# Kernel optimization log

Hardware: AMD Instinct MI355X
Metric: run time of the kernel (lower is better)

Reference implementation:

```python
import jax, jax.numpy as jnp
import numpy as np

DIM = 512
N = 64
DIV = 8
H = DIM // DIV  # 64
BATCH = 8
L_SEQ = 2048


def _kernel_dplr(Lam, P, B, C, step, L):
    # Lam: (N,) complex, P: (N,1), B: (N,H), C: (H,N), step: scalar
    omega = jnp.exp(-2j * jnp.pi * (jnp.arange(L) / L))        # (L,)
    g = (2.0 / step) * (1.0 - omega) / (1.0 + omega)           # (L,) generating-fn nodes
    c = 2.0 / (1.0 + omega)                                    # (L,)
    r = 1.0 / (g[:, None] - Lam[None, :])                      # (L,N) Cauchy resolvent
    Cc = jnp.conj(C)                                           # (H,N)
    p = P[:, 0]                                                # (N,)
    pc = jnp.conj(p)
    # vectorized Cauchy dot-products (torch version loops over L)
    k00 = jnp.einsum('in,nj,ln->lij', Cc, B, r)                # (L,H,H)
    k01 = jnp.einsum('in,n,ln->li', Cc, p, r)                  # (L,H)
    k10 = jnp.einsum('n,nj,ln->lj', pc, B, r)                  # (L,H)
    k11 = jnp.einsum('n,n,ln->l', pc, p, r)                    # (L,)
    # woodbury correction: inv(1 + k11) is a 1x1 batched inverse -> elementwise
    at_roots = c[:, None, None] * (
        k00 - k01[:, :, None] * (1.0 / (1.0 + k11))[:, None, None] * k10[:, None, :]
    )                                                          # (L,H,H)
    return jnp.fft.ifft(at_roots, n=L, axis=0).real            # (L,H,H)


def _fft_conv(u, K):
    # u: (b,L,H) real, K: (L,H,H) real. Linear conv via length-2L FFT.
    L = K.shape[0]
    ud = jnp.fft.rfft(u, n=2 * L, axis=1)                      # (b,Lf,H)
    Kd = jnp.fft.rfft(K, n=2 * L, axis=0)                      # (Lf,H,H)
    yf = jnp.einsum('lij,blj->bli', Kd, ud)                    # (b,Lf,H)
    return jnp.fft.irfft(yf, n=2 * L, axis=1)[:, :L]           # (b,L,H)


def reference(u, Lambda_re, Lambda_im, P_re, P_im, B_re, B_im, C_re, C_im, step):
    # straight-through clamp of Lambda_re (torch does an in-place no_grad clamp)
    Lambda_re = Lambda_re + jax.lax.stop_gradient(
        jnp.minimum(Lambda_re, -1e-4) - Lambda_re)
    Lam = Lambda_re + 1j * Lambda_im                           # (N,div)
    P = P_re + 1j * P_im                                       # (N,1,div)
    Bm = B_re + 1j * B_im                                      # (N,H,div)
    Cm = C_re + 1j * C_im                                      # (H,N,div)
    b, L, d = u.shape
    u4 = u.reshape(b, L, d // DIV, DIV)                        # (b,L,H,div)
    s = jnp.exp(step)[0]
    K = jax.vmap(_kernel_dplr, in_axes=(-1, -1, -1, -1, None, None),
                 out_axes=-1)(Lam, P, Bm, Cm, s, L)            # (L,H,H,div)
    y = jax.vmap(_fft_conv, in_axes=(-1, -1), out_axes=-1)(u4, K)  # (b,L,H,div)
    return y.reshape(b, L, d)


def setup_inputs() -> dict:
    key = jax.random.key(0)
    ks = jax.random.split(key, 10)
    sc = 0.5 ** 0.5
    u = jax.random.normal(ks[0], (BATCH, L_SEQ, DIM), dtype=jnp.float32)
    Lambda_re = -(jax.random.uniform(ks[1], (N, DIV), dtype=jnp.float32) * 0.5 + 0.1)
    Lambda_im = jax.random.normal(ks[2], (N, DIV), dtype=jnp.float32)
    P_re = jax.random.normal(ks[3], (N, 1, DIV), dtype=jnp.float32) * sc
    P_im = jax.random.normal(ks[4], (N, 1, DIV), dtype=jnp.float32) * sc
    B_re = jax.random.normal(ks[5], (N, H, DIV), dtype=jnp.float32) * sc
    B_im = jax.random.normal(ks[6], (N, H, DIV), dtype=jnp.float32) * sc
    C_re = jax.random.normal(ks[7], (H, N, DIV), dtype=jnp.float32) * sc
    C_im = jax.random.normal(ks[8], (H, N, DIV), dtype=jnp.float32) * sc
    step = jax.random.uniform(ks[9], (1,), dtype=jnp.float32,
                              minval=float(np.log(0.001)), maxval=float(np.log(0.1)))
    return {"u": u, "Lambda_re": Lambda_re, "Lambda_im": Lambda_im,
            "P_re": P_re, "P_im": P_im, "B_re": B_re, "B_im": B_im,
            "C_re": C_re, "C_im": C_im, "step": step}
```

## Files before the change

kernel.cpp:

```cpp
#include <hip/hip_runtime.h>
#include <hip/hip_bf16.h>
#include <math.h>

#define LSEQ 2048
#define NM   64
#define HD   64
#define NDIV 8
#define NB   8
#define NF   2049
#define ATROWS 4224

#define SL(E) ((E) + ((E) >> 5))
#define FFT_BUF 2112

typedef __attribute__((ext_vector_type(8))) short bf16x8;
typedef __attribute__((ext_vector_type(4))) float f32x4;

__device__ __forceinline__ unsigned pack_c(float2 v) {
  __hip_bfloat162 h = __float22bfloat162_rn(v);
  return *reinterpret_cast<unsigned*>(&h);
}
__device__ __forceinline__ float2 unpack_c(unsigned u) {
  __hip_bfloat162 h = *reinterpret_cast<__hip_bfloat162*>(&u);
  return __bfloat1622float2(h);
}
__device__ __forceinline__ unsigned short f2bf(float v) {
  __hip_bfloat16 h = __float2bfloat16(v);
  return *reinterpret_cast<unsigned short*>(&h);
}

struct cplxd { double x, y; };
__device__ __forceinline__ cplxd cmuld(cplxd a, cplxd b) {
  return {a.x*b.x - a.y*b.y, a.x*b.y + a.y*b.x};
}
__device__ __forceinline__ cplxd cdivd(cplxd a, cplxd b) {
  double inv = 1.0 / (b.x*b.x + b.y*b.y);
  return {(a.x*b.x + a.y*b.y)*inv, (a.y*b.x - a.x*b.y)*inv};
}

__device__ __forceinline__ void build_tw256(float2* TW) {
  int m = threadIdx.x;
  if (m < 256) {
    float s, c;
    __sincosf(-3.14159265358979324f * (float)m * (1.0f/512.0f), &s, &c);
    TW[m] = make_float2(c, s);
  }
}

template<int SIGN, int M>
__device__ __forceinline__ void r4_stage(const float2* __restrict__ src,
                                         float2* __restrict__ dst,
                                         const float2* __restrict__ TW) {
  constexpr int L = 2048 / (4 * M);
  __syncthreads();
  #pragma unroll
  for (int t = 0; t < 2; t++) {
    int idx = (int)threadIdx.x + t * 256;
    int q = idx / M;
    int p = idx & (M - 1);
    float2 a0 = src[SL(idx)];
    float2 a1 = src[SL(idx + 512)];
    float2 a2 = src[SL(idx + 1024)];
    float2 a3 = src[SL(idx + 1536)];
    float2 w = TW[(p * L) >> 1];
    float2 W1 = make_float2(w.x, (SIGN > 0) ? -w.y : w.y);
    float2 W2 = make_float2(W1.x*W1.x - W1.y*W1.y, 2.f*W1.x*W1.y);
    float2 W3 = make_float2(W2.x*W1.x - W2.y*W1.y, W2.x*W1.y + W2.y*W1.x);
    float2 b1 = make_float2(a1.x*W1.x - a1.y*W1.y, a1.x*W1.y + a1.y*W1.x);
    float2 b2 = make_float2(a2.x*W2.x - a2.y*W2.y, a2.x*W2.y + a2.y*W2.x);
    float2 b3 = make_float2(a3.x*W3.x - a3.y*W3.y, a3.x*W3.y + a3.y*W3.x);
    float2 e0 = make_float2(a0.x + b2.x, a0.y + b2.y);
    float2 e1 = make_float2(b1.x + b3.x, b1.y + b3.y);
    float2 d0 = make_float2(a0.x - b2.x, a0.y - b2.y);
    float2 d1 = make_float2(b1.x - b3.x, b1.y - b3.y);
    float2 o1, o3;
    if (SIGN < 0) { o1 = make_float2(d0.x + d1.y, d0.y - d1.x);
                    o3 = make_float2(d0.x - d1.y, d0.y + d1.x); }
    else          { o1 = make_float2(d0.x - d1.y, d0.y + d1.x);
                    o3 = make_float2(d0.x + d1.y, d0.y - d1.x); }
    int ob = q * 4 * M + p;
    dst[SL(ob)]         = make_float2(e0.x + e1.x, e0.y + e1.y);
    dst[SL(ob + M)]     = o1;
    dst[SL(ob + 2*M)]   = make_float2(e0.x - e1.x, e0.y - e1.y);
    dst[SL(ob + 3*M)]   = o3;
  }
}

template<int SIGN>
__device__ __forceinline__ void r4_mid(float2* a, float2* b, const float2* TW) {
  r4_stage<SIGN,   4>(a, b, TW);
  r4_stage<SIGN,  16>(b, a, TW);
  r4_stage<SIGN,  64>(a, b, TW);
  r4_stage<SIGN, 256>(b, a, TW);
}

template<int SIGN>
__device__ __forceinline__ void r2f_ldst(const float2* __restrict__ src,
                                         float2* __restrict__ dst) {
  __syncthreads();
  #pragma unroll
  for (int t = 0; t < 4; t++) {
    int p = (int)threadIdx.x + t * 256;
    float2 a = src[SL(p)], b = src[SL(p + 1024)];
    float s, c;
    __sincosf(-6.28318530717958647f * (float)p * (1.0f/2048.0f), &s, &c);
    float wy = (SIGN > 0) ? -s : s;
    float2 wb = make_float2(b.x*c - b.y*wy, b.x*wy + b.y*c);
    dst[SL(p)]        = make_float2(a.x + wb.x, a.y + wb.y);
    dst[SL(p + 1024)] = make_float2(a.x - wb.x, a.y - wb.y);
  }
}

__device__ __forceinline__ void r4g_bf16_inv(const unsigned* __restrict__ row,
                                             float2* __restrict__ dst) {
  #pragma unroll
  for (int t = 0; t < 2; t++) {
    int idx = (int)threadIdx.x + t * 256;
    float2 a0 = unpack_c(row[idx]);
    float2 a1 = unpack_c(row[idx + 512]);
    float2 a2 = unpack_c(row[idx + 1024]);
    float2 a3 = unpack_c(row[idx + 1536]);
    float2 e0 = make_float2(a0.x + a2.x, a0.y + a2.y);
    float2 e1 = make_float2(a1.x + a3.x, a1.y + a3.y);
    float2 d0 = make_float2(a0.x - a2.x, a0.y - a2.y);
    float2 d1 = make_float2(a1.x - a3.x, a1.y - a3.y);
    float2 o1 = make_float2(d0.x - d1.y, d0.y + d1.x);
    float2 o3 = make_float2(d0.x + d1.y, d0.y - d1.x);
    int ob = idx * 4;
    dst[SL(ob)]   = make_float2(e0.x + e1.x, e0.y + e1.y);
    dst[SL(ob+1)] = o1;
    dst[SL(ob+2)] = make_float2(e0.x - e1.x, e0.y - e1.y);
    dst[SL(ob+3)] = o3;
  }
}

__device__ __forceinline__ void r4g_f32pad_fwd(const float2* __restrict__ g,
                                               float2* __restrict__ dst) {
  #pragma unroll
  for (int t = 0; t < 2; t++) {
    int idx = (int)threadIdx.x + t * 256;
    float2 a0 = g[idx];
    float2 a1 = g[idx + 512];
    int ob = idx * 4;
    dst[SL(ob)]   = make_float2(a0.x + a1.x, a0.y + a1.y);
    dst[SL(ob+1)] = make_float2(a0.x + a1.y, a0.y - a1.x);
    dst[SL(ob+2)] = make_float2(a0.x - a1.x, a0.y - a1.y);
    dst[SL(ob+3)] = make_float2(a0.x - a1.y, a0.y + a1.x);
  }
}

__device__ __forceinline__ void r4_modstage(const float2* __restrict__ src,
                                            float2* __restrict__ dst) {
  __syncthreads();
  const float sc = 1.0f/2048.0f;
  const float R = 0.70710678118654752f;
  #pragma unroll
  for (int t = 0; t < 2; t++) {
    int idx = (int)threadIdx.x + t * 256;
    float k0 = src[SL(idx)].x        * sc;
    float k1 = src[SL(idx + 512)].x  * sc;
    float k2 = src[SL(idx + 1024)].x * sc;
    float k3 = src[SL(idx + 1536)].x * sc;
    float s, c;
    __sincosf(-3.14159265358979324f * (float)idx * (1.0f/2048.0f), &s, &c);
    float2 a0 = make_float2(k0*c,         k0*s);
    float2 a1 = make_float2(k1*R*(c + s), k1*R*(s - c));
    float2 a2 = make_float2(k2*s,        -k2*c);
    float2 a3 = make_float2(k3*R*(s - c), -k3*R*(s + c));
    float2 e0 = make_float2(a0.x + a2.x, a0.y + a2.y);
    float2 e1 = make_float2(a1.x + a3.x, a1.y + a3.y);
    float2 d0 = make_float2(a0.x - a2.x, a0.y - a2.y);
    float2 d1 = make_float2(a1.x - a3.x, a1.y - a3.y);
    float2 o1 = make_float2(d0.x + d1.y, d0.y - d1.x);
    float2 o3 = make_float2(d0.x - d1.y, d0.y + d1.x);
    int ob = idx * 4;
    dst[SL(ob)]   = make_float2(e0.x + e1.x, e0.y + e1.y);
    dst[SL(ob+1)] = o1;
    dst[SL(ob+2)] = make_float2(e0.x - e1.x, e0.y - e1.y);
    dst[SL(ob+3)] = o3;
  }
}

__device__ __forceinline__ void r2f_gw_bf16(const float2* __restrict__ src,
                                            unsigned* __restrict__ row) {
  __syncthreads();
  #pragma unroll
  for (int t = 0; t < 4; t++) {
    int p = (int)threadIdx.x + t * 256;
    float2 a = src[SL(p)], b = src[SL(p + 1024)];
    float s, c;
    __sincosf(-6.28318530717958647f * (float)p * (1.0f/2048.0f), &s, &c);
    float2 wb = make_float2(b.x*c - b.y*s, b.x*s + b.y*c);
    row[2*p + 1] = pack_c(make_float2(a.x + wb.x, a.y + wb.y));
  }
}

__device__ __forceinline__ void r2f_gw_f32h(const float2* __restrict__ src,
                                            float2* __restrict__ dst) {
  __syncthreads();
  const float sc = 1.0f/2048.0f;
  #pragma unroll
  for (int t = 0; t < 4; t++) {
    int p = (int)threadIdx.x + t * 256;
    float2 a = src[SL(p)], b = src[SL(p + 1024)];
    float s, c;
    __sincosf(-6.28318530717958647f * (float)p * (1.0f/2048.0f), &s, &c);
    float wy = -s;
    float2 wb = make_float2(b.x*c - b.y*wy, b.x*wy + b.y*c);
    dst[p] = make_float2((a.x + wb.x)*sc, (a.y + wb.y)*sc);
  }
}

__global__ __launch_bounds__(256) void ssm_kt(
    const float* __restrict__ Cre, const float* __restrict__ Cim,
    const float* __restrict__ Bre, const float* __restrict__ Bim,
    const float* __restrict__ Pre, const float* __restrict__ Pim,
    float2* __restrict__ CT, float2* __restrict__ BT, float2* __restrict__ PT) {
  int idx = blockIdx.x * 256 + threadIdx.x;
  int dv = idx >> 12, n = (idx >> 6) & 63, x = idx & 63;
  CT[idx] = make_float2(Cre[((size_t)x*NM + n)*NDIV + dv], -Cim[((size_t)x*NM + n)*NDIV + dv]);
  BT[idx] = make_float2(Bre[((size_t)n*HD + x)*NDIV + dv],  Bim[((size_t)n*HD + x)*NDIV + dv]);
  if (idx < NDIV*NM) {
    int dv2 = idx >> 6, n2 = idx & 63;
    PT[idx] = make_float2(Pre[n2*NDIV + dv2], Pim[n2*NDIV + dv2]);
  }
}

__global__ __launch_bounds__(256) void ssm_k0a(
    const float* __restrict__ Lre, const float* __restrict__ Lim,
    const float* __restrict__ Pre, const float* __restrict__ Pim,
    const float* __restrict__ step, unsigned short* __restrict__ RBr,
    unsigned short* __restrict__ RBi, float2* __restrict__ cpx) {
  int idx = blockIdx.x * 256 + threadIdx.x;
  int qn = idx & 3;
  int rest = idx >> 2;
  int l = rest & (LSEQ - 1);
  int dv = rest >> 11;
  double s = (double)expf(step[0]);
  float angf = -6.2831855f * ((float)l * (1.0f/2048.0f));
  double si, co;
  sincos((double)angf, &si, &co);
  cplxd om    = {co, si};
  cplxd one_p = {1.0 + om.x,  om.y};
  double ts = 2.0 / s;
  cplxd g = cdivd({ts*(1.0 - om.x), ts*(-om.y)}, one_p);
  cplxd c = cdivd({2.0, 0.0}, one_p);
  double k11x = 0.0, k11y = 0.0;
  for (int u = 0; u < 16; u++) {
    int n = qn*16 + u;
    float lre = fminf(Lre[n*NDIV+dv], -0.0001f);
    float lim = Lim[n*NDIV+dv];
    cplxd den = {g.x - (double)lre, g.y - (double)lim};
    cplxd r   = cdivd({1.0, 0.0}, den);
    cplxd rcv = cmuld(c, r);
    size_t bidx = (((size_t)(dv*8 + (n >> 3)))*LSEQ + l)*8 + (n & 7);
    RBr[bidx] = f2bf((float)rcv.x);
    RBi[bidx] = f2bf((float)rcv.y);
    double pr = (double)Pre[n*NDIV+dv], pi = (double)Pim[n*NDIV+dv];
    double p2 = pr*pr + pi*pi;
    k11x += p2 * rcv.x; k11y += p2 * rcv.y;
  }
  k11x += __shfl_xor(k11x, 1); k11y += __shfl_xor(k11y, 1);
  k11x += __shfl_xor(k11x, 2); k11y += __shfl_xor(k11y, 2);
  if (qn == 0)
    cpx[(size_t)dv*LSEQ + l] = make_float2((float)(c.x + k11x), (float)(c.y + k11y));
}

__global__ __launch_bounds__(256) void ssm_km(
    const float2* __restrict__ CT, const float2* __restrict__ BT,
    const float2* __restrict__ PT, unsigned short* __restrict__ ATr,
    unsigned short* __restrict__ ATi, unsigned short* __restrict__ ATin) {
  __shared__ float2 PAN[4096];
  __shared__ float2 ROW[64];
  int dv = blockIdx.y;
  int ib = blockIdx.x;
  int tid = threadIdx.x;
  if (ib < 64) {
    for (int q = tid; q < 4096; q += 256) PAN[q] = BT[(size_t)dv*4096 + q];
    if (tid < 64) ROW[tid] = CT[(size_t)dv*4096 + tid*64 + ib];
    __syncthreads();
    int j = tid >> 2, nq = tid & 3;
    size_t rbase = ((size_t)dv*ATROWS + ib*64 + j)*64;
    for (int u = 0; u < 16; u++) {
      int n = nq*16 + u;
      float2 cv = ROW[n];
      float2 bv = PAN[n*64 + j];
      float xr = cv.x*bv.x - cv.y*bv.y, xi = cv.x*bv.y + cv.y*bv.x;
      ATr[rbase + n] = f2bf(xr); ATi[rbase + n] = f2bf(xi); ATin[rbase + n] = f2bf(-xi);
    }
  } else {
    for (int q = tid; q < 4096; q += 256) PAN[q] = CT[(size_t)dv*4096 + q];
    if (tid < 64) ROW[tid] = PT[dv*64 + tid];
    __syncthreads();
    int x = tid >> 2, nq = tid & 3;
    size_t pbase = ((size_t)dv*ATROWS + 4096 + x)*64;
    for (int u = 0; u < 16; u++) {
      int n = nq*16 + u;
      float2 cv = PAN[n*64 + x];
      float2 pv = ROW[n];
      float xr = cv.x*pv.x - cv.y*pv.y, xi = cv.x*pv.y + cv.y*pv.x;
      ATr[pbase + n] = f2bf(xr); ATi[pbase + n] = f2bf(xi); ATin[pbase + n] = f2bf(-xi);
    }
    __syncthreads();
    for (int q = tid; q < 4096; q += 256) PAN[q] = BT[(size_t)dv*4096 + q];
    __syncthreads();
    size_t qbase = ((size_t)dv*ATROWS + 4160 + x)*64;
    for (int u = 0; u < 16; u++) {
      int n = nq*16 + u;
      float2 bv = PAN[n*64 + x];
      float2 pv = ROW[n];
      float xr = pv.x*bv.x + pv.y*bv.y, xi = pv.x*bv.y - pv.y*bv.x;
      ATr[qbase + n] = f2bf(xr); ATi[qbase + n] = f2bf(xi); ATin[qbase + n] = f2bf(-xi);
    }
  }
}

__device__ __forceinline__ void gemm_core(
    const unsigned short* __restrict__ ATr, const unsigned short* __restrict__ ATi,
    const unsigned short* __restrict__ ATin, const unsigned short* __restrict__ RBr,
    const unsigned short* __restrict__ RBi, int dv, int mrow0, int l0, int lane,
    f32x4 accR[4], f32x4 accI[4]) {
  int mloc = lane & 15, kgrp = lane >> 4;
  #pragma unroll
  for (int t = 0; t < 4; t++) {
    accR[t] = (f32x4){0.f, 0.f, 0.f, 0.f};
    accI[t] = (f32x4){0.f, 0.f, 0.f, 0.f};
  }
  size_t abase = ((size_t)dv*ATROWS + mrow0 + mloc)*64 + kgrp*8;
  #pragma unroll
  for (int s = 0; s < 2; s++) {
    bf16x8 ar = *reinterpret_cast<const bf16x8*>(ATr  + abase + s*32);
    bf16x8 ai = *reinterpret_cast<const bf16x8*>(ATi  + abase + s*32);
    bf16x8 an = *reinterpret_cast<const bf16x8*>(ATin + abase + s*32);
    size_t bbase = (((size_t)(dv*8 + s*4 + kgrp))*LSEQ + l0 + mloc)*8;
    #pragma unroll
    for (int t = 0; t < 4; t++) {
      bf16x8 br = *reinterpret_cast<const bf16x8*>(RBr + bbase + t*128);
      bf16x8 bi = *reinterpret_cast<const bf16x8*>(RBi + bbase + t*128);
      accR[t] = __builtin_amdgcn_mfma_f32_16x16x32_bf16(ar, br, accR[t], 0, 0, 0);
      accR[t] = __builtin_amdgcn_mfma_f32_16x16x32_bf16(an, bi, accR[t], 0, 0, 0);
      accI[t] = __builtin_amdgcn_mfma_f32_16x16x32_bf16(ar, bi, accI[t], 0, 0, 0);
      accI[t] = __builtin_amdgcn_mfma_f32_16x16x32_bf16(ai, br, accI[t], 0, 0, 0);
    }
  }
}

__global__ __launch_bounds__(256) void ssm_g1(
    const unsigned short* __restrict__ ATr, const unsigned short* __restrict__ ATi,
    const unsigned short* __restrict__ ATin, const unsigned short* __restrict__ RBr,
    const unsigned short* __restrict__ RBi, const float2* __restrict__ cpx,
    float2* __restrict__ A1h, float2* __restrict__ K10h) {
  int which = blockIdx.x;
  int nBlk = blockIdx.y;
  int dv = blockIdx.z;
  int wave = threadIdx.x >> 6, lane = threadIdx.x & 63;
  int mrow0 = 4096 + which*64 + wave*16;
  int l0 = nBlk * 64;
  f32x4 accR[4], accI[4];
  gemm_core(ATr, ATi, ATin, RBr, RBi, dv, mrow0, l0, lane, accR, accI);
  int rbase = (lane >> 4) * 4;
  #pragma unroll
  for (int t = 0; t < 4; t++) {
    int l = l0 + t*16 + (lane & 15);
    if (which == 0) {
      float2 w = cpx[((size_t)dv << 11) + l];
      float inv = 1.0f / (w.x*w.x + w.y*w.y);
      #pragma unroll
      for (int r = 0; r < 4; r++) {
        int x = wave*16 + rbase + r;
        float sx = accR[t][r], sy = accI[t][r];
        A1h[((size_t)(dv*64 + x))*LSEQ + l] =
            make_float2((sx*w.x + sy*w.y)*inv, (sy*w.x - sx*w.y)*inv);
      }
    } else {
      #pragma unroll
      for (int r = 0; r < 4; r++) {
        int x = wave*16 + rbase + r;
        K10h[((size_t)(dv*LSEQ + l))*64 + x] = make_float2(accR[t][r], accI[t][r]);
      }
    }
  }
}

__global__ __launch_bounds__(256) void ssm_g2(
    const unsigned short* __restrict__ ATr, const unsigned short* __restrict__ ATi,
    const unsigned short* __restrict__ ATin, const unsigned short* __restrict__ RBr,
    const unsigned short* __restrict__ RBi, const float2* __restrict__ A1h,
    const float2* __restrict__ K10h, unsigned* __restrict__ big, int dv) {
  int mBlk = blockIdx.x;
  int nBlk = blockIdx.y;
  int wave = threadIdx.x >> 6, lane = threadIdx.x & 63;
  int mrow0 = mBlk*64 + wave*16;
  int l0 = nBlk * 64;
  f32x4 accR[4], accI[4];
  gemm_core(ATr, ATi, ATin, RBr, RBi, dv, mrow0, l0, lane, accR, accI);
  int rbase = (lane >> 4) * 4;
  #pragma unroll
  for (int t = 0; t < 4; t++) {
    int l = l0 + t*16 + (lane & 15);
    float2 a1 = A1h[((size_t)(dv*64 + mBlk))*LSEQ + l];
    const float2* kp = K10h + ((size_t)(dv*LSEQ + l))*64 + wave*16 + rbase;
    #pragma unroll
    for (int r = 0; r < 4; r++) {
      float2 k10 = kp[r];
      float cx = a1.x*k10.x - a1.y*k10.y;
      float cy = a1.x*k10.y + a1.y*k10.x;
      int chain = mBlk*64 + wave*16 + rbase + r;
      big[(size_t)chain*NF + l] = pack_c(make_float2(accR[t][r] - cx, accI[t][r] - cy));
    }
  }
}

__global__ __launch_bounds__(256) void ssm_ku(const float* __restrict__ u, float* __restrict__ ut) {
  __shared__ float s[16][513];
  int b  = blockIdx.x >> 7;
  int l0 = (blockIdx.x & 127) << 4;
  int tid = threadIdx.x;
  for (int q = tid; q < 16*512; q += 256) {
    int ll = q >> 9, dd = q & 511;
    s[ll][dd] = u[((size_t)b*LSEQ + l0 + ll)*512 + dd];
  }
  __syncthreads();
  for (int q = tid; q < 16*512; q += 256) {
    int d = q >> 4, ll = q & 15;
    int dvv = d & 7, h = d >> 3;
    ut[(((size_t)(dvv*NB + b))*HD + h)*LSEQ + l0 + ll] = s[ll][d];
  }
}

__global__ __launch_bounds__(256) void ssm_k3(const float* __restrict__ ut, float2* __restrict__ ud, int dv) {
  __shared__ float2 b0[FFT_BUF];
  __shared__ float2 b1[FFT_BUF];
  __shared__ float2 TW[256];
  int tid = threadIdx.x;
  int c = blockIdx.x;
  const float2* src = (const float2*)(ut + ((size_t)dv*512 + c) * LSEQ);
  float2* dst = ud + (size_t)c * NF;
  build_tw256(TW);
  r4g_f32pad_fwd(src, b1);
  r4_mid<-1>(b1, b0, TW);
  r2f_ldst<-1>(b1, b0);
  __syncthreads();
  for (int f = tid; f <= 2048; f += 256) {
    int fa = f & 2047, fb = (2048 - f) & 2047;
    float2 Zf = b0[SL(fa)];
    float2 Zm = b0[SL(fb)];
    float Ex = (Zf.x + Zm.x)*0.5f, Ey = (Zf.y - Zm.y)*0.5f;
    float Dx = Zf.x - Zm.x,        Dy = Zf.y + Zm.y;
    float Ox = Dy*0.5f, Oy = -Dx*0.5f;
    float s, c2;
    __sincosf(-6.28318530717958647f * (float)f * (1.0f/4096.0f), &s, &c2);
    float WOx = Ox*c2 - Oy*s, WOy = Ox*s + Oy*c2;
    dst[f] = make_float2(Ex + WOx, Ey + WOy);
  }
}

__global__ __launch_bounds__(256) void ssm_k2(unsigned* __restrict__ big) {
  __shared__ float2 b0[FFT_BUF];
  __shared__ float2 b1[FFT_BUF];
  __shared__ float2 TW[256];
  int tid = threadIdx.x;
  unsigned* row = big + (size_t)blockIdx.x * NF;
  build_tw256(TW);
  float2 ev[4];
  #pragma unroll
  for (int k = 0; k < 4; k++) {
    int l = tid + 256*k;
    float2 a = unpack_c(row[l]);
    float2 b = unpack_c(row[(2048 - l) & 2047]);
    ev[k] = make_float2((a.x + b.x)*0.5f, (a.y - b.y)*0.5f);
  }
  float ev1024 = (tid == 0) ? unpack_c(row[1024]).x : 0.f;
  r4g_bf16_inv(row, b1);
  __syncthreads();
  #pragma unroll
  for (int k = 0; k < 4; k++) { int l = tid + 256*k; row[2*l] = pack_c(ev[k]); }
  if (tid == 0) row[2048] = pack_c(make_float2(ev1024, 0.f));
  r4_mid<1>(b1, b0, TW);
  r2f_ldst<1>(b1, b0);
  r4_modstage(b0, b1);
  r4_mid<-1>(b1, b0, TW);
  r2f_gw_bf16(b1, row);
}

__global__ __launch_bounds__(256) void ssm_k4(
    const unsigned* __restrict__ kdt, const float2* __restrict__ ud,
    float2* __restrict__ yf) {
  __shared__ float2 uds[NB][32][16];
  int tid = threadIdx.x;
  int f0 = blockIdx.x * 16;
  int i0 = blockIdx.y * 16;
  int ii = tid >> 4, ff = tid & 15;
  int i = i0 + ii;
  int f = f0 + ff;
  int fr = (f < NF) ? f : 2048;
  float2 acc[NB];
  #pragma unroll
  for (int b = 0; b < NB; b++) acc[b] = make_float2(0.f, 0.f);
  for (int jh = 0; jh < 2; jh++) {
    __syncthreads();
    for (int q = tid; q < NB*32*16; q += 256) {
      int b = q >> 9, j = (q >> 4) & 31, fq = q & 15;
      int f_ = f0 + fq;
      uds[b][j][fq] = (f_ < NF) ? ud[((size_t)(b*HD + jh*32 + j))*NF + f_]
                                : make_float2(0.f, 0.f);
    }
    __syncthreads();
    for (int j = 0; j < 32; j++) {
      float2 kv = unpack_c(kdt[((size_t)(i*HD + jh*32 + j))*NF + fr]);
      #pragma unroll
      for (int b = 0; b < NB; b++) {
        float2 uv = uds[b][j][ff];
        acc[b].x += kv.x*uv.x - kv.y*uv.y;
        acc[b].y += kv.x*uv.y + kv.y*uv.x;
      }
    }
  }
  if (f < NF) {
    #pragma unroll
    for (int b = 0; b < NB; b++)
      yf[((size_t)(b*HD + i))*NF + f] = acc[b];
  }
}

__global__ __launch_bounds__(256) void ssm_k5(const float2* __restrict__ yf,
                                              float* __restrict__ yt, int dv) {
  __shared__ float2 b0[FFT_BUF];
  __shared__ float2 b1[FFT_BUF];
  __shared__ float2 TW[256];
  int tid = threadIdx.x;
  int b = blockIdx.x >> 6, i = blockIdx.x & 63;
  const float2* src = yf + (size_t)(b*HD + i) * NF;
  float2* dst = (float2*)(yt + (((size_t)(dv*NB + b))*HD + i) * LSEQ);
  build_tw256(TW);
  for (int k = tid; k < 2048; k += 256) {
    float2 Xk = src[k];
    float2 Xm = src[2048 - k];
    float Ex = (Xk.x + Xm.x)*0.5f, Ey = (Xk.y - Xm.y)*0.5f;
    float Dx = Xk.x - Xm.x,        Dy = Xk.y + Xm.y;
    float s, c;
    __sincosf(6.28318530717958647f * (float)k * (1.0f/4096.0f), &s, &c);
    float Ox = 0.5f*(Dx*c - Dy*s);
    float Oy = 0.5f*(Dx*s + Dy*c);
    b0[SL(k)] = make_float2(Ex - Oy, Ey + Ox);
  }
  r4_stage<1, 1>(b0, b1, TW);
  r4_mid<1>(b1, b0, TW);
  r2f_gw_f32h(b1, dst);
}

__global__ __launch_bounds__(256) void ssm_t2(const float* __restrict__ yt, float* __restrict__ out) {
  __shared__ float s[512][17];
  int b  = blockIdx.x >> 7;
  int t0 = (blockIdx.x & 127) << 4;
  int tid = threadIdx.x;
  for (int q = tid; q < 512*16; q += 256) {
    int d = q >> 4, tt = q & 15;
    int dvv = d & 7, i = d >> 3;
    s[d][tt] = yt[(((size_t)(dvv*NB + b))*HD + i)*LSEQ + t0 + tt];
  }
  __syncthreads();
  for (int q = tid; q < 512*16; q += 256) {
    int tt = q >> 9, d = q & 511;
    out[((size_t)b*LSEQ + t0 + tt)*512 + d] = s[d][tt];
  }
}

extern "C" void kernel_launch(void* const* d_in, const int* in_sizes, int n_in,
                              void* d_out, int out_size, void* d_ws, size_t ws_size,
                              hipStream_t stream) {
  const float* u    = (const float*)d_in[0];
  const float* Lre  = (const float*)d_in[1];
  const float* Lim  = (const float*)d_in[2];
  const float* Pre  = (const float*)d_in[3];
  const float* Pim  = (const float*)d_in[4];
  const float* Bre  = (const float*)d_in[5];
  const float* Bim  = (const float*)d_in[6];
  const float* Cre  = (const float*)d_in[7];
  const float* Cim  = (const float*)d_in[8];
  const float* step = (const float*)d_in[9];
  float* out = (float*)d_out;

  char* w = (char*)d_ws;
  size_t off = 0;
  auto carve = [&](size_t bytes) -> void* {
    void* p = (void*)(w + off);
    off += (bytes + 255) & ~(size_t)255;
    return p;
  };
  float2*   cpx  = (float2*)carve((size_t)NDIV*LSEQ*sizeof(float2));
  float*    ut   = (float*) carve((size_t)NDIV*NB*HD*LSEQ*sizeof(float));
  unsigned* big  = (unsigned*)carve((size_t)4096*NF*sizeof(unsigned));
  float2*   ud   = (float2*)carve((size_t)512*NF*sizeof(float2));
  float2*   yf   = (float2*)carve((size_t)512*NF*sizeof(float2));
  float2*   CT   = (float2*)carve((size_t)NDIV*NM*HD*sizeof(float2));
  float2*   BT   = (float2*)carve((size_t)NDIV*NM*HD*sizeof(float2));
  float2*   PT   = (float2*)carve((size_t)NDIV*NM*sizeof(float2));
  unsigned short* ATr  = (unsigned short*)carve((size_t)NDIV*ATROWS*64*2);
  unsigned short* ATi  = (unsigned short*)carve((size_t)NDIV*ATROWS*64*2);
  unsigned short* ATin = (unsigned short*)carve((size_t)NDIV*ATROWS*64*2);
  unsigned short* RBr  = (unsigned short*)carve((size_t)NDIV*8*LSEQ*8*2);
  unsigned short* RBi  = (unsigned short*)carve((size_t)NDIV*8*LSEQ*8*2);
  float2*   A1h  = (float2*)carve((size_t)NDIV*64*LSEQ*sizeof(float2));
  float2*   K10h = (float2*)carve((size_t)NDIV*LSEQ*64*sizeof(float2));
  (void)in_sizes; (void)n_in; (void)out_size;
  if (ws_size < off) return;

  ssm_kt<<<128, 256, 0, stream>>>(Cre, Cim, Bre, Bim, Pre, Pim, CT, BT, PT);
  ssm_k0a<<<256, 256, 0, stream>>>(Lre, Lim, Pre, Pim, step, RBr, RBi, cpx);
  ssm_km<<<dim3(65, 8), 256, 0, stream>>>(CT, BT, PT, ATr, ATi, ATin);
  ssm_ku<<<1024, 256, 0, stream>>>(u, ut);
  ssm_g1<<<dim3(2, 32, 8), 256, 0, stream>>>(ATr, ATi, ATin, RBr, RBi, cpx, A1h, K10h);
  for (int dv = 0; dv < NDIV; ++dv) {
    ssm_k3<<<512, 256, 0, stream>>>(ut, ud, dv);
    ssm_g2<<<dim3(64, 32), 256, 0, stream>>>(ATr, ATi, ATin, RBr, RBi, A1h, K10h, big, dv);
    ssm_k2<<<4096, 256, 0, stream>>>(big);
    ssm_k4<<<dim3(129, 4), 256, 0, stream>>>(big, ud, yf);
    ssm_k5<<<512, 256, 0, stream>>>(yf, ut, dv);
  }
  ssm_t2<<<1024, 256, 0, stream>>>(ut, out);
}
```

Measured before the change: 1.022 ms.

## Compute FFT twiddles inline, fuse radix-2 into mod stage, batch input FFTs

```diff
diff --git a/kernel.cpp b/kernel.cpp
--- a/kernel.cpp
+++ b/kernel.cpp
@@ -10,8 +10,8 @@
 #define NF   2049
 #define ATROWS 4224
 
-#define SL(E) ((E) + ((E) >> 5))
-#define FFT_BUF 2112
+#define SL(E) ((E) + ((E) >> 3))
+#define FFT_BUF 2304
 
 typedef __attribute__((ext_vector_type(8))) short bf16x8;
 typedef __attribute__((ext_vector_type(4))) float f32x4;
@@ -38,19 +38,9 @@
   return {(a.x*b.x + a.y*b.y)*inv, (a.y*b.x - a.x*b.y)*inv};
 }
 
-__device__ __forceinline__ void build_tw256(float2* TW) {
-  int m = threadIdx.x;
-  if (m < 256) {
-    float s, c;
-    __sincosf(-3.14159265358979324f * (float)m * (1.0f/512.0f), &s, &c);
-    TW[m] = make_float2(c, s);
-  }
-}
-
 template<int SIGN, int M>
 __device__ __forceinline__ void r4_stage(const float2* __restrict__ src,
-                                         float2* __restrict__ dst,
-                                         const float2* __restrict__ TW) {
+                                         float2* __restrict__ dst) {
   constexpr int L = 2048 / (4 * M);
   __syncthreads();
   #pragma unroll
@@ -62,13 +52,17 @@
     float2 a1 = src[SL(idx + 512)];
     float2 a2 = src[SL(idx + 1024)];
     float2 a3 = src[SL(idx + 1536)];
-    float2 w = TW[(p * L) >> 1];
-    float2 W1 = make_float2(w.x, (SIGN > 0) ? -w.y : w.y);
-    float2 W2 = make_float2(W1.x*W1.x - W1.y*W1.y, 2.f*W1.x*W1.y);
-    float2 W3 = make_float2(W2.x*W1.x - W2.y*W1.y, W2.x*W1.y + W2.y*W1.x);
-    float2 b1 = make_float2(a1.x*W1.x - a1.y*W1.y, a1.x*W1.y + a1.y*W1.x);
-    float2 b2 = make_float2(a2.x*W2.x - a2.y*W2.y, a2.x*W2.y + a2.y*W2.x);
-    float2 b3 = make_float2(a3.x*W3.x - a3.y*W3.y, a3.x*W3.y + a3.y*W3.x);
+    float2 b1, b2, b3;
+    if constexpr (M > 1) {
+      float s, c;
+      __sincosf(-3.14159265358979324f * (float)(p * L) * (1.0f/1024.0f), &s, &c);
+      float2 W1 = make_float2(c, (SIGN > 0) ? -s : s);
+      float2 W2 = make_float2(W1.x*W1.x - W1.y*W1.y, 2.f*W1.x*W1.y);
+      float2 W3 = make_float2(W2.x*W1.x - W2.y*W1.y, W2.x*W1.y + W2.y*W1.x);
+      b1 = make_float2(a1.x*W1.x - a1.y*W1.y, a1.x*W1.y + a1.y*W1.x);
+      b2 = make_float2(a2.x*W2.x - a2.y*W2.y, a2.x*W2.y + a2.y*W2.x);
+      b3 = make_float2(a3.x*W3.x - a3.y*W3.y, a3.x*W3.y + a3.y*W3.x);
+    } else { b1 = a1; b2 = a2; b3 = a3; }
     float2 e0 = make_float2(a0.x + b2.x, a0.y + b2.y);
     float2 e1 = make_float2(b1.x + b3.x, b1.y + b3.y);
     float2 d0 = make_float2(a0.x - b2.x, a0.y - b2.y);
@@ -87,11 +81,11 @@
 }
 
 template<int SIGN>
-__device__ __forceinline__ void r4_mid(float2* a, float2* b, const float2* TW) {
-  r4_stage<SIGN,   4>(a, b, TW);
-  r4_stage<SIGN,  16>(b, a, TW);
-  r4_stage<SIGN,  64>(a, b, TW);
-  r4_stage<SIGN, 256>(b, a, TW);
+__device__ __forceinline__ void r4_mid(float2* a, float2* b) {
+  r4_stage<SIGN,   4>(a, b);
+  r4_stage<SIGN,  16>(b, a);
+  r4_stage<SIGN,  64>(a, b);
+  r4_stage<SIGN, 256>(b, a);
 }
 
 template<int SIGN>
@@ -149,7 +143,7 @@
   }
 }
 
-__device__ __forceinline__ void r4_modstage(const float2* __restrict__ src,
+__device__ __forceinline__ void r4_modfused(const float2* __restrict__ pre,
                                             float2* __restrict__ dst) {
   __syncthreads();
   const float sc = 1.0f/2048.0f;
@@ -157,10 +151,19 @@
   #pragma unroll
   for (int t = 0; t < 2; t++) {
     int idx = (int)threadIdx.x + t * 256;
-    float k0 = src[SL(idx)].x        * sc;
-    float k1 = src[SL(idx + 512)].x  * sc;
-    float k2 = src[SL(idx + 1024)].x * sc;
-    float k3 = src[SL(idx + 1536)].x * sc;
+    float a0x = pre[SL(idx)].x;
+    float a1x = pre[SL(idx + 512)].x;
+    float2 bA = pre[SL(idx + 1024)];
+    float2 bB = pre[SL(idx + 1536)];
+    float sA, cA, sB, cB;
+    __sincosf(-6.28318530717958647f * (float)idx * (1.0f/2048.0f), &sA, &cA);
+    __sincosf(-6.28318530717958647f * (float)(idx + 512) * (1.0f/2048.0f), &sB, &cB);
+    float rA = bA.x*cA + bA.y*sA;
+    float rB = bB.x*cB + bB.y*sB;
+    float k0 = (a0x + rA) * sc;
+    float k1 = (a1x + rB) * sc;
+    float k2 = (a0x - rA) * sc;
+    float k3 = (a1x - rB) * sc;
     float s, c;
     __sincosf(-3.14159265358979324f * (float)idx * (1.0f/2048.0f), &s, &c);
     float2 a0 = make_float2(k0*c,         k0*s);
@@ -428,17 +431,15 @@
   }
 }
 
-__global__ __launch_bounds__(256) void ssm_k3(const float* __restrict__ ut, float2* __restrict__ ud, int dv) {
+__global__ __launch_bounds__(256) void ssm_k3(const float* __restrict__ ut,
+                                              float2* __restrict__ ud, int cbase) {
   __shared__ float2 b0[FFT_BUF];
   __shared__ float2 b1[FFT_BUF];
-  __shared__ float2 TW[256];
   int tid = threadIdx.x;
-  int c = blockIdx.x;
-  const float2* src = (const float2*)(ut + ((size_t)dv*512 + c) * LSEQ);
-  float2* dst = ud + (size_t)c * NF;
-  build_tw256(TW);
+  const float2* src = (const float2*)(ut + ((size_t)(cbase + blockIdx.x)) * LSEQ);
+  float2* dst = ud + (size_t)blockIdx.x * NF;
   r4g_f32pad_fwd(src, b1);
-  r4_mid<-1>(b1, b0, TW);
+  r4_mid<-1>(b1, b0);
   r2f_ldst<-1>(b1, b0);
   __syncthreads();
   for (int f = tid; f <= 2048; f += 256) {
@@ -458,10 +459,8 @@
 __global__ __launch_bounds__(256) void ssm_k2(unsigned* __restrict__ big) {
   __shared__ float2 b0[FFT_BUF];
   __shared__ float2 b1[FFT_BUF];
-  __shared__ float2 TW[256];
   int tid = threadIdx.x;
   unsigned* row = big + (size_t)blockIdx.x * NF;
-  build_tw256(TW);
   float2 ev[4];
   #pragma unroll
   for (int k = 0; k < 4; k++) {
@@ -476,11 +475,10 @@
   #pragma unroll
   for (int k = 0; k < 4; k++) { int l = tid + 256*k; row[2*l] = pack_c(ev[k]); }
   if (tid == 0) row[2048] = pack_c(make_float2(ev1024, 0.f));
-  r4_mid<1>(b1, b0, TW);
-  r2f_ldst<1>(b1, b0);
-  r4_modstage(b0, b1);
-  r4_mid<-1>(b1, b0, TW);
-  r2f_gw_bf16(b1, row);
+  r4_mid<1>(b1, b0);
+  r4_modfused(b1, b0);
+  r4_mid<-1>(b0, b1);
+  r2f_gw_bf16(b0, row);
 }
 
 __global__ __launch_bounds__(256) void ssm_k4(
@@ -527,12 +525,10 @@
                                               float* __restrict__ yt, int dv) {
   __shared__ float2 b0[FFT_BUF];
   __shared__ float2 b1[FFT_BUF];
-  __shared__ float2 TW[256];
   int tid = threadIdx.x;
   int b = blockIdx.x >> 6, i = blockIdx.x & 63;
   const float2* src = yf + (size_t)(b*HD + i) * NF;
   float2* dst = (float2*)(yt + (((size_t)(dv*NB + b))*HD + i) * LSEQ);
-  build_tw256(TW);
   for (int k = tid; k < 2048; k += 256) {
     float2 Xk = src[k];
     float2 Xm = src[2048 - k];
@@ -544,8 +540,8 @@
     float Oy = 0.5f*(Dx*s + Dy*c);
     b0[SL(k)] = make_float2(Ex - Oy, Ey + Ox);
   }
-  r4_stage<1, 1>(b0, b1, TW);
-  r4_mid<1>(b1, b0, TW);
+  r4_stage<1, 1>(b0, b1);
+  r4_mid<1>(b1, b0);
   r2f_gw_f32h(b1, dst);
 }
 
@@ -591,7 +587,6 @@
   float2*   cpx  = (float2*)carve((size_t)NDIV*LSEQ*sizeof(float2));
   float*    ut   = (float*) carve((size_t)NDIV*NB*HD*LSEQ*sizeof(float));
   unsigned* big  = (unsigned*)carve((size_t)4096*NF*sizeof(unsigned));
-  float2*   ud   = (float2*)carve((size_t)512*NF*sizeof(float2));
   float2*   yf   = (float2*)carve((size_t)512*NF*sizeof(float2));
   float2*   CT   = (float2*)carve((size_t)NDIV*NM*HD*sizeof(float2));
   float2*   BT   = (float2*)carve((size_t)NDIV*NM*HD*sizeof(float2));
@@ -603,19 +598,29 @@
   unsigned short* RBi  = (unsigned short*)carve((size_t)NDIV*8*LSEQ*8*2);
   float2*   A1h  = (float2*)carve((size_t)NDIV*64*LSEQ*sizeof(float2));
   float2*   K10h = (float2*)carve((size_t)NDIV*LSEQ*64*sizeof(float2));
+  size_t off_m = off;
+  float2* ud_full = (float2*)carve((size_t)NDIV*512*NF*sizeof(float2));
+  bool full = (ws_size >= off);
+  float2* ud = ud_full;
+  if (!full) {
+    off = off_m;
+    ud = (float2*)carve((size_t)512*NF*sizeof(float2));
+    if (ws_size < off) return;
+  }
   (void)in_sizes; (void)n_in; (void)out_size;
-  if (ws_size < off) return;
 
   ssm_kt<<<128, 256, 0, stream>>>(Cre, Cim, Bre, Bim, Pre, Pim, CT, BT, PT);
   ssm_k0a<<<256, 256, 0, stream>>>(Lre, Lim, Pre, Pim, step, RBr, RBi, cpx);
   ssm_km<<<dim3(65, 8), 256, 0, stream>>>(CT, BT, PT, ATr, ATi, ATin);
   ssm_ku<<<1024, 256, 0, stream>>>(u, ut);
   ssm_g1<<<dim3(2, 32, 8), 256, 0, stream>>>(ATr, ATi, ATin, RBr, RBi, cpx, A1h, K10h);
+  if (full) ssm_k3<<<4096, 256, 0, stream>>>(ut, ud_full, 0);
   for (int dv = 0; dv < NDIV; ++dv) {
-    ssm_k3<<<512, 256, 0, stream>>>(ut, ud, dv);
+    if (!full) ssm_k3<<<512, 256, 0, stream>>>(ut, ud, dv*512);
+    const float2* udp = full ? (ud_full + (size_t)dv*512*NF) : ud;
     ssm_g2<<<dim3(64, 32), 256, 0, stream>>>(ATr, ATi, ATin, RBr, RBi, A1h, K10h, big, dv);
     ssm_k2<<<4096, 256, 0, stream>>>(big);
-    ssm_k4<<<dim3(129, 4), 256, 0, stream>>>(big, ud, yf);
+    ssm_k4<<<dim3(129, 4), 256, 0, stream>>>(big, udp, yf);
     ssm_k5<<<512, 256, 0, stream>>>(yf, ut, dv);
   }
   ssm_t2<<<1024, 256, 0, stream>>>(ut, out);
```

New measurement: 951.6 us. 1.07x faster.
